# Optimization experiments

Hardware: AMD Instinct MI355X
Metric: run time of the kernel (lower is better)

Reference implementation:

```python
import math
import jax, jax.numpy as jnp
import numpy as np

D_K = 1024


def setup_inputs() -> dict:
    key = jax.random.key(0)
    ks = jax.random.split(key, 7)
    B, L, d_model, d_k = 8, 2048, 1024, D_K
    source = jax.random.normal(ks[0], (B, L, d_model), dtype=jnp.float32)
    # torch nn.Linear params: weight (out, in), bias (out,)
    Wq = jax.random.normal(ks[1], (d_k, d_model), dtype=jnp.float32) * 0.02
    Wk = jax.random.normal(ks[2], (d_k, d_model), dtype=jnp.float32) * 0.02
    Wv = jax.random.normal(ks[3], (d_k, d_model), dtype=jnp.float32) * 0.02
    bq = jnp.zeros((d_k,), dtype=jnp.float32)
    bk = jnp.zeros((d_k,), dtype=jnp.float32)
    bv = jnp.zeros((d_k,), dtype=jnp.float32)
    return {"source": source, "Wq": Wq, "bq": bq, "Wk": Wk, "bk": bk,
            "Wv": Wv, "bv": bv, "mask": 1}


def reference(source, Wq, bq, Wk, bk, Wv, bv, mask):
    # q,k,v: (B, L, d_k); torch Linear => x @ W.T + b
    q = jnp.einsum("bld,kd->blk", source, Wq) + bq
    k = jnp.einsum("bld,kd->blk", source, Wk) + bk
    v = jnp.einsum("bld,kd->blk", source, Wv) + bv  # target defaults to source
    L = source.shape[1]
    scores = jnp.einsum("blk,bmk->blm", q, k) / math.sqrt(D_K)  # (B, L, L)
    if mask:
        # -inf strictly above the diagonal (j > i)
        causal = jnp.triu(jnp.full((L, L), -jnp.inf, dtype=scores.dtype), k=1)
        scores = scores + causal
    # Faithful to original: Softmax(dim=1) -> normalize over axis 1 (rows)
    attention = jax.nn.softmax(scores, axis=1)
    output = jnp.einsum("blm,bmk->blk", attention, v)  # (B, L, d_k)
    return (output, attention)
```

## Files before the change

kernel.cpp:

```cpp
#include <hip/hip_runtime.h>
#include <hip/hip_bf16.h>

typedef __attribute__((ext_vector_type(8))) __bf16 bf16x8;
typedef __attribute__((ext_vector_type(8))) unsigned short us8;
typedef __attribute__((ext_vector_type(4))) float f32x4;
typedef long long ll;

#define GLD(gp, lp) __builtin_amdgcn_global_load_lds( \
    (const __attribute__((address_space(1))) void*)(gp), \
    (__attribute__((address_space(3))) void*)(lp), 16, 0, 0)

#define SBAR()  asm volatile("s_barrier" ::: "memory")
#define VMCNT4  asm volatile("s_waitcnt vmcnt(4)" ::: "memory")
#define VMCNT0  asm volatile("s_waitcnt vmcnt(0)" ::: "memory")
#define SCHED0() __builtin_amdgcn_sched_barrier(0)

template<int OP>
__global__ __launch_bounds__(512) void gemm8(
    const __bf16* __restrict__ A, const __bf16* __restrict__ B,
    void* __restrict__ Cp, const float* __restrict__ bias,
    const int* __restrict__ maskp, float* __restrict__ part,
    int K, int lda, int ldb, int ldc,
    ll batchA, ll batchB, ll batchC)
{
    __shared__ __bf16 LA[2][256][64];
    __shared__ __bf16 LB[2][256][64];

    const int bx = blockIdx.x, by = blockIdx.y, bz = blockIdx.z;
    const int t    = threadIdx.x;
    const int w    = t >> 6, lane = t & 63;
    const int wrm  = w >> 2, wcn  = w & 3;
    const int fr   = lane & 15, fq = lane >> 4;
    const int row0 = bx * 256;
    const int col0 = by * 256;
    const int msk  = (OP >= 1) ? maskp[0] : 0;

    if (OP == 1 && msk && by > bx) {
        __bf16* C = (__bf16*)Cp + (ll)bz * batchC;
        bf16x8 z = {};
        #pragma unroll 4
        for (int pass = 0; pass < 16; ++pass) {
            int r = pass * 16 + (t >> 5);
            *(bf16x8*)&C[(ll)(row0 + r) * ldc + col0 + (t & 31) * 8] = z;
        }
        if (part && t < 256) part[((ll)bx * 8 + bz) * 2048 + col0 + t] = 0.f;
        return;
    }

    int NT = K / 64;
    if (OP == 2 && msk) NT = (row0 + 256) / 64;
    const int NI = NT / 2;

    const __bf16* Ab = A + (ll)bz * batchA;
    const __bf16* Bb = B + (ll)bz * batchB;

    const int srow = lane >> 3;
    const int cg   = (lane & 7) ^ srow;

    auto stageA = [&](int kt, int h, int slot) {
        #pragma unroll
        for (int is = 0; is < 2; ++is)
            GLD(Ab + (ll)(row0 + h*128 + is*64 + w*8 + srow) * lda + kt*64 + cg*8,
                &LA[slot][h*128 + is*64 + w*8][0]);
    };
    auto stageB = [&](int kt, int h, int slot) {
        #pragma unroll
        for (int is = 0; is < 2; ++is)
            GLD(Bb + (ll)(col0 + h*128 + is*64 + w*8 + srow) * ldb + kt*64 + cg*8,
                &LB[slot][h*128 + is*64 + w*8][0]);
    };
    auto rdA = [&](int slot, int row, int g) -> bf16x8 {
        return *(const bf16x8*)&LA[slot][row][(g ^ (row & 7)) << 3];
    };
    auto rdB = [&](int slot, int row, int g) -> bf16x8 {
        return *(const bf16x8*)&LB[slot][row][(g ^ (row & 7)) << 3];
    };

    f32x4  acc[8][4] = {};
    bf16x8 bB[4][2];

    stageA(0, 0, 0); stageA(0, 1, 0);
    stageB(0, 0, 0); stageB(0, 1, 0);
    stageB(1, 0, 1); stageB(1, 1, 1);
    VMCNT4;
    SBAR();

#define PHASE(SLOT, Q, STG, VMC) \
  { \
    if (Q == 0) { \
      _Pragma("unroll") for (int j = 0; j < 4; ++j) \
      _Pragma("unroll") for (int ks = 0; ks < 2; ++ks) \
        bB[j][ks] = rdB(SLOT, wcn*64 + j*16 + fr, ks*4 + fq); \
    } \
    bf16x8 bA[2][2]; \
    _Pragma("unroll") for (int fi = 0; fi < 2; ++fi) \
    _Pragma("unroll") for (int ks = 0; ks < 2; ++ks) \
      bA[fi][ks] = rdA(SLOT, wrm*128 + (Q*2+fi)*16 + fr, ks*4 + fq); \
    STG; \
    VMC; \
    SBAR(); SCHED0(); \
    __builtin_amdgcn_s_setprio(1); \
    _Pragma("unroll") for (int fi = 0; fi < 2; ++fi) \
    _Pragma("unroll") for (int j = 0; j < 4; ++j) \
    _Pragma("unroll") for (int ks = 0; ks < 2; ++ks) \
      acc[Q*2+fi][j] = __builtin_amdgcn_mfma_f32_16x16x32_bf16( \
          bA[fi][ks], bB[j][ks], acc[Q*2+fi][j], 0, 0, 0); \
    __builtin_amdgcn_s_setprio(0); \
    SCHED0(); SBAR(); \
  }

    for (int i = 0; i < NI; ++i) {
        const bool nl = (i < NI - 1);
        const int k1 = 2*i + 1, k2 = 2*i + 2, k3 = 2*i + 3;
        PHASE(0, 0, stageA(k1, 0, 1), );
        PHASE(0, 1, stageA(k1, 1, 1), );
        PHASE(0, 2, if (nl) stageB(k2, 0, 0), );
        PHASE(0, 3, if (nl) stageB(k2, 1, 0), if (nl) { VMCNT4; } else { VMCNT0; });
        PHASE(1, 0, if (nl) stageA(k2, 0, 0), );
        PHASE(1, 1, if (nl) stageA(k2, 1, 0), );
        PHASE(1, 2, if (nl) stageB(k3, 0, 1), );
        PHASE(1, 3, if (nl) stageB(k3, 1, 1), if (nl) { VMCNT4; });
    }
#undef PHASE

    const ll coff = (ll)bz * batchC;
    float s4[4] = {0.f, 0.f, 0.f, 0.f};
    #pragma unroll
    for (int fi = 0; fi < 8; ++fi)
    #pragma unroll
    for (int j = 0; j < 4; ++j)
    #pragma unroll
    for (int r4 = 0; r4 < 4; ++r4) {
        const int row = row0 + wrm*128 + fi*16 + fq*4 + r4;
        const int col = col0 + wcn*64 + j*16 + fr;
        float v = acc[fi][j][r4];
        if (OP == 0) {
            v += bias[col];
            ((__bf16*)Cp)[coff + (ll)row * ldc + col] = (__bf16)v;
        } else if (OP == 1) {
            float e = (msk && col > row) ? 0.f : __expf(v * 0.03125f);
            __bf16 eb = (__bf16)e;
            ((__bf16*)Cp)[coff + (ll)row * ldc + col] = eb;
            s4[j] += (float)eb;
        } else {
            ((float*)Cp)[coff + (ll)row * ldc + col] = v;
        }
    }
    if (OP == 1 && part != nullptr) {
        float* red = (float*)&LA[0][0][0];
        __syncthreads();
        #pragma unroll
        for (int j = 0; j < 4; ++j)
            red[(wrm*4 + fq)*256 + wcn*64 + j*16 + fr] = s4[j];
        __syncthreads();
        if (t < 256) {
            float tot = 0.f;
            #pragma unroll
            for (int r = 0; r < 8; ++r) tot += red[r*256 + t];
            part[((ll)bx * 8 + bz) * 2048 + col0 + t] = tot;
        }
    }
}

__global__ __launch_bounds__(256) void cvt_k(const float* __restrict__ in,
                                             __bf16* __restrict__ out, int n8)
{
    const int i = blockIdx.x * 256 + threadIdx.x;
    if (i >= n8) return;
    const f32x4* p = (const f32x4*)(in + (ll)i * 8);
    f32x4 a = p[0], b = p[1];
    bf16x8 h;
    #pragma unroll
    for (int j = 0; j < 4; ++j) { h[j] = (__bf16)a[j]; h[j + 4] = (__bf16)b[j]; }
    *(bf16x8*)(out + (ll)i * 8) = h;
}

__global__ __launch_bounds__(256) void cvtb_k(const float* __restrict__ q,
                                              const float* __restrict__ k,
                                              const float* __restrict__ v,
                                              float* __restrict__ bb)
{
    const int i = blockIdx.x * 256 + threadIdx.x;
    bb[i] = (i < 1024) ? q[i] : (i < 2048) ? k[i - 1024] : v[i - 2048];
}

__global__ __launch_bounds__(256) void rsum_k(const float* __restrict__ part,
                                              float* __restrict__ inv)
{
    const int idx = blockIdx.x * 256 + threadIdx.x;
    const int b = idx >> 11, m = idx & 2047;
    float s = 0.f;
    #pragma unroll
    for (int lc = 0; lc < 8; ++lc) s += part[((ll)lc * 8 + b) * 2048 + m];
    inv[idx] = 1.0f / s;
}

__global__ __launch_bounds__(256) void vtp_k(const __bf16* __restrict__ qkv,
                                             const float* __restrict__ inv,
                                             __bf16* __restrict__ vt)
{
    __shared__ __bf16 tile[64][72];
    const int t  = threadIdx.x;
    const int m0 = blockIdx.x * 64;
    const int k0 = blockIdx.y * 64;
    const int b  = blockIdx.z;

    const __bf16* V = qkv + (ll)b * 2048 * 3072 + 2048;
    #pragma unroll
    for (int h = 0; h < 2; ++h) {
        int r = (t >> 3) + h * 32;
        int c = (t & 7) * 8;
        int m = m0 + r;
        const float iv = inv[b * 2048 + m];
        bf16x8 v = *(const bf16x8*)&V[(ll)m * 3072 + k0 + c];
        bf16x8 o;
        #pragma unroll
        for (int j = 0; j < 8; ++j) o[j] = (__bf16)((float)v[j] * iv);
        *(bf16x8*)&tile[r][c] = o;
    }
    __syncthreads();
    __bf16* O = vt + (ll)b * 1024 * 2048;
    #pragma unroll
    for (int h = 0; h < 2; ++h) {
        int k = (t >> 3) + h * 32;
        int m = (t & 7) * 8;
        bf16x8 o;
        #pragma unroll
        for (int j = 0; j < 8; ++j) o[j] = tile[m + j][k];
        *(bf16x8*)&O[(ll)(k0 + k) * 2048 + m0 + m] = o;
    }
}

__global__ __launch_bounds__(256) void vt_k(const unsigned short* __restrict__ qkv,
                                            unsigned short* __restrict__ vt)
{
    __shared__ unsigned short tile[64][72];
    const int t  = threadIdx.x;
    const int m0 = blockIdx.x * 64;
    const int k0 = blockIdx.y * 64;
    const int b  = blockIdx.z;

    const unsigned short* V = qkv + (ll)b * 2048 * 3072 + 2048;
    #pragma unroll
    for (int h = 0; h < 2; ++h) {
        int r = (t >> 3) + h * 32;
        int c = (t & 7) * 8;
        us8 v = *(const us8*)&V[(ll)(m0 + r) * 3072 + k0 + c];
        *(us8*)&tile[r][c] = v;
    }
    __syncthreads();
    unsigned short* O = vt + (ll)b * 1024 * 2048;
    #pragma unroll
    for (int h = 0; h < 2; ++h) {
        int k = (t >> 3) + h * 32;
        int m = (t & 7) * 8;
        us8 o;
        #pragma unroll
        for (int j = 0; j < 8; ++j) o[j] = tile[m + j][k];
        *(us8*)&O[(ll)(k0 + k) * 2048 + m0 + m] = o;
    }
}

__global__ __launch_bounds__(256) void norm2_k(const __bf16* __restrict__ E,
                                               const float* __restrict__ inv,
                                               float* __restrict__ attn)
{
    const int lc = blockIdx.x, mc = blockIdx.y, b = blockIdx.z;
    const int m  = mc * 256 + threadIdx.x;
    const float iv = inv[b * 2048 + m];
    const __bf16* p = E + (ll)b * 2048 * 2048 + (ll)(lc * 256) * 2048 + m;
    float* qo = attn + (ll)b * 2048 * 2048 + (ll)(lc * 256) * 2048 + m;
    #pragma unroll 4
    for (int l = 0; l < 256; ++l)
        qo[(ll)l * 2048] = (float)p[(ll)l * 2048] * iv;
}

__global__ __launch_bounds__(256) void colsum_k(const __bf16* __restrict__ E,
                                                float* __restrict__ part)
{
    const int lc = blockIdx.x, mc = blockIdx.y, b = blockIdx.z;
    const int m  = mc * 256 + threadIdx.x;
    const __bf16* p = E + (ll)b * 2048 * 2048 + (ll)(lc * 256) * 2048 + m;
    float s = 0.f;
    #pragma unroll 4
    for (int l = 0; l < 256; ++l) s += (float)p[(ll)l * 2048];
    part[((ll)lc * 8 + b) * 2048 + m] = s;
}

__global__ __launch_bounds__(256) void norm_k(const __bf16* __restrict__ E,
                                              const float* __restrict__ part,
                                              float* __restrict__ attn,
                                              __bf16* __restrict__ attn_bf)
{
    const int lc = blockIdx.x, mc = blockIdx.y, b = blockIdx.z;
    const int m  = mc * 256 + threadIdx.x;
    float s = 0.f;
    #pragma unroll
    for (int j = 0; j < 8; ++j) s += part[((ll)j * 8 + b) * 2048 + m];
    const float iv = 1.0f / s;
    const __bf16* p = E + (ll)b * 2048 * 2048 + (ll)(lc * 256) * 2048 + m;
    float*  qo = attn    + (ll)b * 2048 * 2048 + (ll)(lc * 256) * 2048 + m;
    __bf16* ro = attn_bf + (ll)b * 2048 * 2048 + (ll)(lc * 256) * 2048 + m;
    #pragma unroll 4
    for (int l = 0; l < 256; ++l) {
        float a = (float)p[(ll)l * 2048] * iv;
        qo[(ll)l * 2048] = a;
        ro[(ll)l * 2048] = (__bf16)a;
    }
}

extern "C" void kernel_launch(void* const* d_in, const int* in_sizes, int n_in,
                              void* d_out, int out_size, void* d_ws, size_t ws_size,
                              hipStream_t stream)
{
    const float* X   = (const float*)d_in[0];
    const float* Wq  = (const float*)d_in[1];
    const float* bq  = (const float*)d_in[2];
    const float* Wk  = (const float*)d_in[3];
    const float* bk  = (const float*)d_in[4];
    const float* Wv  = (const float*)d_in[5];
    const float* bv  = (const float*)d_in[6];
    const int*   msk = (const int*)d_in[7];

    float* out  = (float*)d_out;
    float* attn = out + (ll)8 * 2048 * 1024;

    __bf16* Xb = (__bf16*)attn;
    __bf16* Wb = Xb + (ll)16384 * 1024;
    float*  bb = (float*)(Wb + (ll)3072 * 1024);

    __bf16* qkv = (__bf16*)d_ws;
    __bf16* vt  = qkv + (ll)16384 * 3072;

    cvt_k<<<dim3(8192), 256, 0, stream>>>(X, Xb, 16384 * 1024 / 8);
    cvt_k<<<dim3(512),  256, 0, stream>>>(Wq, Wb,               1024 * 1024 / 8);
    cvt_k<<<dim3(512),  256, 0, stream>>>(Wk, Wb + 1024 * 1024, 1024 * 1024 / 8);
    cvt_k<<<dim3(512),  256, 0, stream>>>(Wv, Wb + 2048 * 1024, 1024 * 1024 / 8);
    cvtb_k<<<dim3(12),  256, 0, stream>>>(bq, bk, bv, bb);

    gemm8<0><<<dim3(64, 12, 1), 512, 0, stream>>>(
        Xb, Wb, qkv, bb, msk, nullptr,
        1024, 1024, 1024, 3072, 0LL, 0LL, 0LL);

    const size_t need_fused =
        (size_t)(16384ll*3072 + 8ll*1024*2048 + 8ll*2048*2048) * 2
        + (size_t)(8*8*2048 + 8*2048) * 4;

    if (ws_size >= need_fused) {
        __bf16* E   = vt + (ll)8 * 1024 * 2048;
        float*  prt = (float*)(E + (ll)8 * 2048 * 2048);
        float*  inv = prt + 8 * 8 * 2048;

        gemm8<1><<<dim3(8, 8, 8), 512, 0, stream>>>(
            qkv, qkv + 1024, E, nullptr, msk, prt,
            1024, 3072, 3072, 2048,
            (ll)2048 * 3072, (ll)2048 * 3072, (ll)2048 * 2048);

        rsum_k<<<dim3(64), 256, 0, stream>>>(prt, inv);

        vtp_k<<<dim3(32, 16, 8), 256, 0, stream>>>(qkv, inv, vt);

        norm2_k<<<dim3(8, 8, 8), 256, 0, stream>>>(E, inv, attn);

        gemm8<2><<<dim3(8, 4, 8), 512, 0, stream>>>(
            E, vt, out, nullptr, msk, nullptr,
            2048, 2048, 2048, 1024,
            (ll)2048 * 2048, (ll)1024 * 2048, (ll)2048 * 1024);
    } else {
        __bf16* E   = (__bf16*)d_out;
        float*  prt = (float*)(vt + (ll)8 * 1024 * 2048);
        __bf16* attn_bf = qkv;

        vt_k<<<dim3(32, 16, 8), 256, 0, stream>>>((const unsigned short*)qkv,
                                                  (unsigned short*)vt);

        gemm8<1><<<dim3(8, 8, 8), 512, 0, stream>>>(
            qkv, qkv + 1024, E, nullptr, msk, nullptr,
            1024, 3072, 3072, 2048,
            (ll)2048 * 3072, (ll)2048 * 3072, (ll)2048 * 2048);

        colsum_k<<<dim3(8, 8, 8), 256, 0, stream>>>(E, prt);
        norm_k<<<dim3(8, 8, 8), 256, 0, stream>>>(E, prt, attn, attn_bf);

        gemm8<2><<<dim3(8, 4, 8), 512, 0, stream>>>(
            attn_bf, vt, out, nullptr, msk, nullptr,
            2048, 2048, 2048, 1024,
            (ll)2048 * 2048, (ll)1024 * 2048, (ll)2048 * 1024);
    }
}
```

Baseline: 358.7 us.

## Fuse attention normalization into a new 128-row PV GEMM kernel

Replaces the separate norm2_k pass and the generic gemm8<2> PV GEMM with one pv128 kernel. The kernel uses 128x256 tiles with a reversed block order so the longer causal rows are scheduled first, and skips K-tiles above the diagonal. After the MMA loop it writes the fp32 attention rows for its tile by scaling E with the inverse column sums. This removes one launch and a strided, column-wise normalization pass, and improves load balance across the causal triangle. In exchange each block carries an extra streaming write at the end, and the smaller tiles may reduce reuse.

```diff
diff --git a/kernel.cpp b/kernel.cpp
--- a/kernel.cpp
+++ b/kernel.cpp
@@ -162,6 +162,129 @@
     }
 }
 
+__global__ __launch_bounds__(512) void pv128(
+    const __bf16* __restrict__ E, const __bf16* __restrict__ VT,
+    const float* __restrict__ inv, float* __restrict__ out,
+    float* __restrict__ attn, const int* __restrict__ maskp)
+{
+    __shared__ __bf16 LA[2][128][64];
+    __shared__ __bf16 LB[2][256][64];
+
+    const int bxr = (int)gridDim.x - 1 - (int)blockIdx.x;
+    const int by = blockIdx.y, bz = blockIdx.z;
+    const int t = threadIdx.x, w = t >> 6, lane = t & 63;
+    const int wrm = w >> 2, wcn = w & 3;
+    const int fr = lane & 15, fq = lane >> 4;
+    const int row0 = bxr * 128, col0 = by * 256;
+    const int msk = maskp[0];
+
+    const int NT = msk ? (row0 + 128) / 64 : 32;
+    const int NI = NT / 2;
+
+    const __bf16* Ab = E  + (ll)bz * 2048 * 2048;
+    const __bf16* Bb = VT + (ll)bz * 1024 * 2048;
+
+    const int srow = lane >> 3;
+    const int cg   = (lane & 7) ^ srow;
+
+    auto stageA = [&](int kt, int slot) {
+        #pragma unroll
+        for (int is = 0; is < 2; ++is)
+            GLD(Ab + (ll)(row0 + is*64 + w*8 + srow) * 2048 + kt*64 + cg*8,
+                &LA[slot][is*64 + w*8][0]);
+    };
+    auto stageB = [&](int kt, int h, int slot) {
+        #pragma unroll
+        for (int is = 0; is < 2; ++is)
+            GLD(Bb + (ll)(col0 + h*128 + is*64 + w*8 + srow) * 2048 + kt*64 + cg*8,
+                &LB[slot][h*128 + is*64 + w*8][0]);
+    };
+    auto rdA = [&](int slot, int row, int g) -> bf16x8 {
+        return *(const bf16x8*)&LA[slot][row][(g ^ (row & 7)) << 3];
+    };
+    auto rdB = [&](int slot, int row, int g) -> bf16x8 {
+        return *(const bf16x8*)&LB[slot][row][(g ^ (row & 7)) << 3];
+    };
+
+    f32x4  acc[4][4] = {};
+    bf16x8 bB[4][2];
+
+    stageA(0, 0); stageB(0, 0, 0); stageB(0, 1, 0);
+    stageB(1, 0, 1); stageB(1, 1, 1);
+    VMCNT4;
+    SBAR();
+
+#define PHASEP(SLOT, Q, STG, VMC) \
+  { \
+    if (Q == 0) { \
+      _Pragma("unroll") for (int j = 0; j < 4; ++j) \
+      _Pragma("unroll") for (int ks = 0; ks < 2; ++ks) \
+        bB[j][ks] = rdB(SLOT, wcn*64 + j*16 + fr, ks*4 + fq); \
+    } \
+    bf16x8 bA[2][2]; \
+    _Pragma("unroll") for (int fi = 0; fi < 2; ++fi) \
+    _Pragma("unroll") for (int ks = 0; ks < 2; ++ks) \
+      bA[fi][ks] = rdA(SLOT, wrm*64 + (Q*2+fi)*16 + fr, ks*4 + fq); \
+    STG; \
+    VMC; \
+    SBAR(); SCHED0(); \
+    __builtin_amdgcn_s_setprio(1); \
+    _Pragma("unroll") for (int fi = 0; fi < 2; ++fi) \
+    _Pragma("unroll") for (int j = 0; j < 4; ++j) \
+    _Pragma("unroll") for (int ks = 0; ks < 2; ++ks) \
+      acc[Q*2+fi][j] = __builtin_amdgcn_mfma_f32_16x16x32_bf16( \
+          bA[fi][ks], bB[j][ks], acc[Q*2+fi][j], 0, 0, 0); \
+    __builtin_amdgcn_s_setprio(0); \
+    SCHED0(); SBAR(); \
+  }
+
+    for (int i = 0; i < NI; ++i) {
+        const bool nl = (i < NI - 1);
+        const int kb = 2*i + 1, ka2 = 2*i + 2, kb2 = 2*i + 3;
+        PHASEP(0, 0, stageA(kb, 1), );
+        PHASEP(0, 1, if (nl) { stageB(ka2, 0, 0); stageB(ka2, 1, 0); },
+                     if (nl) { VMCNT4; } else { VMCNT0; });
+        PHASEP(1, 0, if (nl) stageA(ka2, 0), );
+        PHASEP(1, 1, if (nl) { stageB(kb2, 0, 1); stageB(kb2, 1, 1); },
+                     if (nl) { VMCNT4; });
+    }
+#undef PHASEP
+
+    #pragma unroll
+    for (int qf = 0; qf < 4; ++qf)
+    #pragma unroll
+    for (int j = 0; j < 4; ++j)
+    #pragma unroll
+    for (int r4 = 0; r4 < 4; ++r4) {
+        const int row = row0 + wrm*64 + qf*16 + fq*4 + r4;
+        const int col = col0 + wcn*64 + j*16 + fr;
+        out[(ll)bz*2048*1024 + (ll)row*1024 + col] = acc[qf][j][r4];
+    }
+
+    {
+        const int c0 = by * 512;
+        const int ct = (t & 63) * 8;
+        float iv[8];
+        #pragma unroll
+        for (int e = 0; e < 8; ++e) iv[e] = inv[bz*2048 + c0 + ct + e];
+        const int r00 = t >> 6;
+        #pragma unroll 2
+        for (int ri = 0; ri < 16; ++ri) {
+            const int row = row0 + ri*8 + r00;
+            bf16x8 ev = *(const bf16x8*)&Ab[(ll)row*2048 + c0 + ct];
+            f32x4 lo, hi;
+            #pragma unroll
+            for (int e = 0; e < 4; ++e) {
+                lo[e] = (float)ev[e]     * iv[e];
+                hi[e] = (float)ev[e + 4] * iv[e + 4];
+            }
+            float* ao = attn + (ll)bz*2048*2048 + (ll)row*2048 + c0 + ct;
+            ((f32x4*)ao)[0] = lo;
+            ((f32x4*)ao)[1] = hi;
+        }
+    }
+}
+
 __global__ __launch_bounds__(256) void cvt_k(const float* __restrict__ in,
                                              __bf16* __restrict__ out, int n8)
 {
@@ -259,20 +382,6 @@
         for (int j = 0; j < 8; ++j) o[j] = tile[m + j][k];
         *(us8*)&O[(ll)(k0 + k) * 2048 + m0 + m] = o;
     }
-}
-
-__global__ __launch_bounds__(256) void norm2_k(const __bf16* __restrict__ E,
-                                               const float* __restrict__ inv,
-                                               float* __restrict__ attn)
-{
-    const int lc = blockIdx.x, mc = blockIdx.y, b = blockIdx.z;
-    const int m  = mc * 256 + threadIdx.x;
-    const float iv = inv[b * 2048 + m];
-    const __bf16* p = E + (ll)b * 2048 * 2048 + (ll)(lc * 256) * 2048 + m;
-    float* qo = attn + (ll)b * 2048 * 2048 + (ll)(lc * 256) * 2048 + m;
-    #pragma unroll 4
-    for (int l = 0; l < 256; ++l)
-        qo[(ll)l * 2048] = (float)p[(ll)l * 2048] * iv;
 }
 
 __global__ __launch_bounds__(256) void colsum_k(const __bf16* __restrict__ E,
@@ -360,12 +469,7 @@
 
         vtp_k<<<dim3(32, 16, 8), 256, 0, stream>>>(qkv, inv, vt);
 
-        norm2_k<<<dim3(8, 8, 8), 256, 0, stream>>>(E, inv, attn);
-
-        gemm8<2><<<dim3(8, 4, 8), 512, 0, stream>>>(
-            E, vt, out, nullptr, msk, nullptr,
-            2048, 2048, 2048, 1024,
-            (ll)2048 * 2048, (ll)1024 * 2048, (ll)2048 * 1024);
+        pv128<<<dim3(16, 4, 8), 512, 0, stream>>>(E, vt, inv, out, attn, msk);
     } else {
         __bf16* E   = (__bf16*)d_out;
         float*  prt = (float*)(vt + (ll)8 * 1024 * 2048);
```

Result: faster. 335.9 us (-6.4%).

## Replace P@V GEMM with causal-aware direct-load MFMA kernel and zero-fill masked tiles

Applied to the files above, without the earlier changes.

Swaps the tiled LDS-based gemm8<2> for the attention-times-V product for a lightweight kernel. Each block handles 16 rows and loops only up to the causal boundary, loading operands straight from global memory into MFMA instructions. The normalisation kernel now writes zeros for fully masked upper tiles instead of reading E for them. This aims to cut wasted work above the diagonal, at the cost of losing LDS reuse of the V tiles and relying on cache hits for repeated global loads.

```diff
diff --git a/kernel.cpp b/kernel.cpp
--- a/kernel.cpp
+++ b/kernel.cpp
@@ -162,6 +162,67 @@
     }
 }
 
+__global__ __launch_bounds__(256) void pvlite(
+    const __bf16* __restrict__ E, const __bf16* __restrict__ VT,
+    float* __restrict__ out, const int* __restrict__ maskp)
+{
+    const int r16 = (int)gridDim.x - 1 - (int)blockIdx.x;
+    const int bz  = blockIdx.z;
+    const int t   = threadIdx.x, w = t >> 6, lane = t & 63;
+    const int fr  = lane & 15, fq = lane >> 4;
+    const int row0 = r16 * 16;
+    const int c0   = w * 256;
+    const int msk  = maskp[0];
+
+    const int kmax = msk ? ((row0 + 16 + 31) & ~31) : 2048;
+
+    const __bf16* Eb = E  + (ll)bz * 2048 * 2048 + (ll)(row0 + fr) * 2048 + fq * 8;
+    const __bf16* Vb = VT + (ll)bz * 1024 * 2048 + fq * 8;
+
+    f32x4 acc[16] = {};
+
+    for (int k0 = 0; k0 < kmax; k0 += 32) {
+        bf16x8 a = *(const bf16x8*)(Eb + k0);
+        #pragma unroll
+        for (int j = 0; j < 16; ++j) {
+            bf16x8 b = *(const bf16x8*)(Vb + (ll)(c0 + j*16 + fr) * 2048 + k0);
+            acc[j] = __builtin_amdgcn_mfma_f32_16x16x32_bf16(a, b, acc[j], 0, 0, 0);
+        }
+    }
+
+    float* ob = out + (ll)bz * 2048 * 1024;
+    #pragma unroll
+    for (int j = 0; j < 16; ++j)
+    #pragma unroll
+    for (int r4 = 0; r4 < 4; ++r4) {
+        const int row = row0 + fq*4 + r4;
+        const int col = c0 + j*16 + fr;
+        ob[(ll)row * 1024 + col] = acc[j][r4];
+    }
+}
+
+__global__ __launch_bounds__(256) void norm2m_k(const __bf16* __restrict__ E,
+                                                const float* __restrict__ inv,
+                                                float* __restrict__ attn,
+                                                const int* __restrict__ maskp)
+{
+    const int lc = blockIdx.x, mc = blockIdx.y, b = blockIdx.z;
+    const int m  = mc * 256 + threadIdx.x;
+    float* qo = attn + (ll)b * 2048 * 2048 + (ll)(lc * 256) * 2048 + m;
+
+    if (maskp[0] && mc > lc) {
+        #pragma unroll 4
+        for (int l = 0; l < 256; ++l)
+            qo[(ll)l * 2048] = 0.f;
+        return;
+    }
+    const float iv = inv[b * 2048 + m];
+    const __bf16* p = E + (ll)b * 2048 * 2048 + (ll)(lc * 256) * 2048 + m;
+    #pragma unroll 4
+    for (int l = 0; l < 256; ++l)
+        qo[(ll)l * 2048] = (float)p[(ll)l * 2048] * iv;
+}
+
 __global__ __launch_bounds__(256) void cvt_k(const float* __restrict__ in,
                                              __bf16* __restrict__ out, int n8)
 {
@@ -259,20 +320,6 @@
         for (int j = 0; j < 8; ++j) o[j] = tile[m + j][k];
         *(us8*)&O[(ll)(k0 + k) * 2048 + m0 + m] = o;
     }
-}
-
-__global__ __launch_bounds__(256) void norm2_k(const __bf16* __restrict__ E,
-                                               const float* __restrict__ inv,
-                                               float* __restrict__ attn)
-{
-    const int lc = blockIdx.x, mc = blockIdx.y, b = blockIdx.z;
-    const int m  = mc * 256 + threadIdx.x;
-    const float iv = inv[b * 2048 + m];
-    const __bf16* p = E + (ll)b * 2048 * 2048 + (ll)(lc * 256) * 2048 + m;
-    float* qo = attn + (ll)b * 2048 * 2048 + (ll)(lc * 256) * 2048 + m;
-    #pragma unroll 4
-    for (int l = 0; l < 256; ++l)
-        qo[(ll)l * 2048] = (float)p[(ll)l * 2048] * iv;
 }
 
 __global__ __launch_bounds__(256) void colsum_k(const __bf16* __restrict__ E,
@@ -360,12 +407,9 @@
 
         vtp_k<<<dim3(32, 16, 8), 256, 0, stream>>>(qkv, inv, vt);
 
-        norm2_k<<<dim3(8, 8, 8), 256, 0, stream>>>(E, inv, attn);
-
-        gemm8<2><<<dim3(8, 4, 8), 512, 0, stream>>>(
-            E, vt, out, nullptr, msk, nullptr,
-            2048, 2048, 2048, 1024,
-            (ll)2048 * 2048, (ll)1024 * 2048, (ll)2048 * 1024);
+        norm2m_k<<<dim3(8, 8, 8), 256, 0, stream>>>(E, inv, attn, msk);
+
+        pvlite<<<dim3(128, 1, 8), 256, 0, stream>>>(E, vt, out, msk);
     } else {
         __bf16* E   = (__bf16*)d_out;
         float*  prt = (float*)(vt + (ll)8 * 1024 * 2048);
```

New measurement: 815.1 us. 2.27x slower.
